# Kernel tuning notes

Hardware: AMD Instinct MI355X
Metric: run time of the kernel (lower is better)

Reference implementation:

```python
import jax, jax.numpy as jnp
import numpy as np

DIM = 2048
N_HEADS = 16
N_KV_HEADS = 8
HEAD_DIM = DIM // N_HEADS  # 128
N_REP = N_HEADS // N_KV_HEADS  # 2
HIDDEN = 4 * DIM  # Project hidden dim
SEQ = 2048
BSZ = 2
ROPE_THETA = 10000.0
NEG_INF = -1e9


def setup_inputs() -> dict:
    key = jax.random.key(0)
    ks = jax.random.split(key, 10)
    s_in = 1.0 / np.sqrt(DIM)
    s_hid = 1.0 / np.sqrt(HIDDEN)
    x = jax.random.normal(ks[0], (BSZ, SEQ, DIM), jnp.float32)
    wq = jax.random.normal(ks[1], (DIM, N_HEADS * HEAD_DIM), jnp.float32) * s_in
    wk_w1 = jax.random.normal(ks[2], (DIM, HIDDEN), jnp.float32) * s_in
    wk_w2 = jax.random.normal(ks[3], (HIDDEN, N_KV_HEADS * HEAD_DIM), jnp.float32) * s_hid
    wk_w3 = jax.random.normal(ks[4], (DIM, HIDDEN), jnp.float32) * s_in
    wv_w1 = jax.random.normal(ks[5], (DIM, HIDDEN), jnp.float32) * s_in
    wv_w2 = jax.random.normal(ks[6], (HIDDEN, N_KV_HEADS * HEAD_DIM), jnp.float32) * s_hid
    wv_w3 = jax.random.normal(ks[7], (DIM, HIDDEN), jnp.float32) * s_in
    wo = jax.random.normal(ks[8], (N_HEADS * HEAD_DIM, DIM), jnp.float32) * s_in
    # RoPE tables: angle[t, j] = t * theta^(-2j/head_dim), j in [0, head_dim/2)
    inv_freq = 1.0 / (ROPE_THETA ** (np.arange(0, HEAD_DIM, 2, dtype=np.float64) / HEAD_DIM))
    ang = np.outer(np.arange(SEQ, dtype=np.float64), inv_freq)
    freqs_cos = jnp.asarray(np.cos(ang), jnp.float32)  # [SEQ, HEAD_DIM//2]
    freqs_sin = jnp.asarray(np.sin(ang), jnp.float32)
    # causal additive mask [1, 1, SEQ, SEQ]
    mask = jnp.triu(jnp.full((SEQ, SEQ), NEG_INF, jnp.float32), k=1)[None, None]
    return {
        "x": x, "wq": wq,
        "wk_w1": wk_w1, "wk_w2": wk_w2, "wk_w3": wk_w3,
        "wv_w1": wv_w1, "wv_w2": wv_w2, "wv_w3": wv_w3,
        "wo": wo, "freqs_cos": freqs_cos, "freqs_sin": freqs_sin,
        "mask": mask, "start_pos": 0,
    }


def _rope(x, cos, sin):
    # x: [b, s, h, d]; pairs (x[2j], x[2j+1]) rotated as complex multiply
    xr = x[..., 0::2]
    xi = x[..., 1::2]
    c = cos[None, :, None, :]
    s = sin[None, :, None, :]
    out_r = xr * c - xi * s
    out_i = xr * s + xi * c
    return jnp.stack([out_r, out_i], axis=-1).reshape(x.shape)


def _project(x, w1, w2, w3):
    # SwiGLU-style projection: w2(silu(x@w1) * (x@w3))
    return (jax.nn.silu(x @ w1) * (x @ w3)) @ w2


def reference(x, wq, wk_w1, wk_w2, wk_w3, wv_w1, wv_w2, wv_w3, wo,
              freqs_cos, freqs_sin, mask, start_pos):
    b, s, _ = x.shape
    q = (x @ wq).reshape(b, s, N_HEADS, HEAD_DIM)
    q = _rope(q, freqs_cos, freqs_sin)
    k = _project(x, wk_w1, wk_w2, wk_w3).reshape(b, s, N_KV_HEADS, HEAD_DIM)
    v = _project(x, wv_w1, wv_w2, wv_w3).reshape(b, s, N_KV_HEADS, HEAD_DIM)
    k = _rope(k, freqs_cos, freqs_sin)
    o_keys, o_values = k, v  # is_training=True path: cache is just current k/v
    # repeat_kv (GQA) -> [b, h, s, d]
    kr = jnp.repeat(k, N_REP, axis=2).transpose(0, 2, 1, 3)
    vr = jnp.repeat(v, N_REP, axis=2).transpose(0, 2, 1, 3)
    qt = q.transpose(0, 2, 1, 3)
    scores = jnp.einsum('bhqd,bhkd->bhqk', qt, kr) / np.sqrt(HEAD_DIM).astype(np.float32)
    scores = scores + mask
    attn = jax.nn.softmax(scores.astype(jnp.float32), axis=-1).astype(qt.dtype)
    out = jnp.einsum('bhqk,bhkd->bhqd', attn, vr)
    out = out.transpose(0, 2, 1, 3).reshape(b, s, N_HEADS * HEAD_DIM)
    return (out @ wo, o_keys, o_values)
```

## Files before the change

### kernel.cpp

```cpp
#include <hip/hip_runtime.h>

typedef unsigned short ushort_t;
typedef __attribute__((ext_vector_type(4))) float f32x4;
typedef __attribute__((ext_vector_type(8))) __bf16 bf16x8;
typedef __attribute__((ext_vector_type(4))) unsigned short ushort4_t;
typedef __attribute__((ext_vector_type(8))) unsigned short ushort8_t;
typedef __attribute__((ext_vector_type(2))) unsigned int u32x2;

#define AS1 __attribute__((address_space(1)))
#define AS3 __attribute__((address_space(3)))

__device__ __forceinline__ float bf2f(ushort_t u) {
  unsigned int v = ((unsigned int)u) << 16;
  return __builtin_bit_cast(float, v);
}
__device__ __forceinline__ ushort_t f2bf(float f) {
  unsigned int u = __builtin_bit_cast(unsigned int, f);
  u += 0x7fffu + ((u >> 16) & 1u);
  return (ushort_t)(u >> 16);
}
__device__ __forceinline__ void storeC(float* p, float v) { *p = v; }
__device__ __forceinline__ void storeC(ushort_t* p, float v) { *p = f2bf(v); }

__global__ __launch_bounds__(256) void cast_f32_bf16(const float* __restrict__ in,
                                                     ushort_t* __restrict__ outp) {
  size_t i = ((size_t)blockIdx.x * 256 + threadIdx.x) * 4;
  f32x4 v = *(const f32x4*)(const void*)&in[i];
  ushort4_t o;
#pragma unroll
  for (int j = 0; j < 4; ++j) o[j] = f2bf(v[j]);
  *(ushort4_t*)(void*)&outp[i] = o;
}

__global__ __launch_bounds__(256) void transpose_cast_b(
    const float* __restrict__ W0, const float* __restrict__ W1,
    const float* __restrict__ W2, const float* __restrict__ W3,
    ushort_t* __restrict__ Wt, int K, int N, long long strT) {
  __shared__ float tile[32][33];
  const int z = blockIdx.z;
  const float* W = (z == 0) ? W0 : (z == 1) ? W1 : (z == 2) ? W2 : W3;
  ushort_t* out = Wt + (size_t)(strT * z);
  int n0 = blockIdx.x * 32, k0 = blockIdx.y * 32;
  int tx = threadIdx.x, ty = threadIdx.y;
#pragma unroll
  for (int i = 0; i < 4; ++i)
    tile[ty + 8 * i][tx] = W[(size_t)(k0 + ty + 8 * i) * N + n0 + tx];
  __syncthreads();
#pragma unroll
  for (int i = 0; i < 4; ++i)
    out[(size_t)(n0 + ty + 8 * i) * K + k0 + tx] = f2bf(tile[tx][ty + 8 * i]);
}

__global__ __launch_bounds__(256) void silu_mul(ushort_t* __restrict__ h1,
                                                const ushort_t* __restrict__ h3) {
  size_t i = ((size_t)blockIdx.x * 256 + threadIdx.x) * 8;
  ushort8_t a = *(const ushort8_t*)(const void*)&h1[i];
  ushort8_t b = *(const ushort8_t*)(const void*)&h3[i];
#pragma unroll
  for (int j = 0; j < 8; ++j) {
    float x = bf2f(a[j]);
    float g = x / (1.0f + __expf(-x));
    a[j] = f2bf(g * bf2f(b[j]));
  }
  *(ushort8_t*)(void*)&h1[i] = a;
}

__global__ __launch_bounds__(256) void reduce_q(const float* __restrict__ part,
                                                ushort_t* __restrict__ qb,
                                                const float* __restrict__ fc,
                                                const float* __restrict__ fs) {
  const float alpha = 0.08838834764831845f;
  int p = blockIdx.x * 256 + threadIdx.x;
  int i = p & 63;
  int row = p >> 10;
  int s = row & 2047;
  size_t src = (size_t)row * 2048 + ((p >> 6) & 15) * 128 + 2 * i;
  float xr = part[src] + part[src + 8388608];
  float xi = part[src + 1] + part[src + 8388609];
  float c = fc[s * 64 + i] * alpha, sn = fs[s * 64 + i] * alpha;
  qb[src] = f2bf(xr * c - xi * sn);
  qb[src + 1] = f2bf(xr * sn + xi * c);
}

__global__ __launch_bounds__(256) void reduce_k(const float* __restrict__ part,
                                                ushort_t* __restrict__ kb,
                                                float* __restrict__ okeys,
                                                const float* __restrict__ fc,
                                                const float* __restrict__ fs) {
  int p = blockIdx.x * 256 + threadIdx.x;
  int i = p & 63;
  int row = p >> 9;
  int s = row & 2047;
  size_t src = (size_t)row * 1024 + ((p >> 6) & 7) * 128 + 2 * i;
  float xr = part[src] + part[src + 4194304] + part[src + 8388608] + part[src + 12582912];
  float xi = part[src + 1] + part[src + 1 + 4194304] + part[src + 1 + 8388608] +
             part[src + 1 + 12582912];
  float c = fc[s * 64 + i], sn = fs[s * 64 + i];
  float orr = xr * c - xi * sn;
  float oi = xr * sn + xi * c;
  kb[src] = f2bf(orr);
  kb[src + 1] = f2bf(oi);
  okeys[src] = orr;
  okeys[src + 1] = oi;
}

__global__ __launch_bounds__(256) void reduce_v(const float* __restrict__ part,
                                                float* __restrict__ ovals,
                                                ushort_t* __restrict__ vbT) {
  __shared__ ushort_t tile[32][33];
  int s0 = blockIdx.x * 32, d0 = blockIdx.y * 32, bk = blockIdx.z;
  int b = bk >> 3, kh = bk & 7;
  int tx = threadIdx.x, ty = threadIdx.y;
#pragma unroll
  for (int i = 0; i < 4; ++i) {
    int s = s0 + ty + 8 * i;
    size_t src = ((size_t)(b * 2048 + s)) * 1024 + kh * 128 + d0 + tx;
    float v = part[src] + part[src + 4194304] + part[src + 8388608] + part[src + 12582912];
    tile[ty + 8 * i][tx] = f2bf(v);
    ovals[src] = v;
  }
  __syncthreads();
#pragma unroll
  for (int i = 0; i < 4; ++i) {
    int d = d0 + ty + 8 * i;
    vbT[((size_t)bk * 128 + d) * 2048 + s0 + tx] = tile[tx][ty + 8 * i];
  }
}

__global__ __launch_bounds__(256) void reduce_wo(const float* __restrict__ part,
                                                 float* __restrict__ outp) {
  size_t i = ((size_t)blockIdx.x * 256 + threadIdx.x) * 4;
  f32x4 a = *(const f32x4*)(const void*)&part[i];
  f32x4 b = *(const f32x4*)(const void*)&part[i + 8388608];
  *(f32x4*)(void*)&outp[i] = a + b;
}

__global__ __launch_bounds__(256) void flash_attn(
    const ushort_t* __restrict__ Q, const ushort_t* __restrict__ Kg,
    const ushort_t* __restrict__ VT, ushort_t* __restrict__ O) {
  __shared__ __align__(16) char smem[81920];
  const int xp = blockIdx.x;
  const int bh = blockIdx.y;
  const int b = bh >> 4, h = bh & 15, kh = h >> 1;
  const int t = threadIdx.x, w = t >> 6, lane = t & 63;
  const int fr = lane & 15, fh = lane >> 4;
  const size_t kelem0 = ((size_t)b * 2048) * 1024 + kh * 128;
  const size_t velem0 = ((size_t)(b * 8 + kh)) * 128 * 2048;
  const size_t qrow0 = (size_t)b * 2048;

  size_t oK[4], oV[4];
#pragma unroll
  for (int qv = 0; qv < 4; ++qv) {
    int row = w * 16 + qv * 4 + (lane >> 4);
    oK[qv] = (size_t)row * 1024 + (((lane & 15) ^ (row & 7)) * 8);
    int rd = w * 32 + qv * 8 + (lane >> 3);
    oV[qv] = (size_t)rd * 2048 + (((lane & 7) ^ (rd & 7)) * 8);
  }

  auto stage = [&](int tile, int buf) {
    const size_t kc = (size_t)tile * 64 * 1024;
    const int vc = tile * 64;
    char* kd = smem + buf * 16384 + w * 4096;
    char* vd = smem + 32768 + buf * 16384 + w * 4096;
#pragma unroll
    for (int qv = 0; qv < 4; ++qv) {
      __builtin_amdgcn_global_load_lds((const AS1 void*)(Kg + kelem0 + kc + oK[qv]),
                                       (AS3 void*)(kd + qv * 1024), 16, 0, 0);
      __builtin_amdgcn_global_load_lds((const AS1 void*)(VT + velem0 + oV[qv] + vc),
                                       (AS3 void*)(vd + qv * 1024), 16, 0, 0);
    }
  };

#pragma unroll 1
  for (int ph = 0; ph < 2; ++ph) {
    const int qi = ph ? (15 - xp) : xp;
    const int qw = qi * 128 + w * 32;
    const int nt = 2 * qi + 2;

    bf16x8 qF[2][4];
#pragma unroll
    for (int qt = 0; qt < 2; ++qt)
#pragma unroll
      for (int i = 0; i < 4; ++i)
        qF[qt][i] = *(const bf16x8*)(const void*)(
            Q + (qrow0 + qw + qt * 16 + fr) * 2048 + h * 128 + i * 32 + fh * 8);

    f32x4 acco[8][2] = {};
    float mrun[2] = {-1e30f, -1e30f};
    float lrun[2] = {0.0f, 0.0f};

    stage(0, 0);
#pragma unroll 1
    for (int tt = 0; tt < nt; ++tt) {
      const int c0 = tt * 64;
      if (tt + 1 < nt) {
        stage(tt + 1, (tt + 1) & 1);
        asm volatile("s_waitcnt vmcnt(8)" ::: "memory");
      } else {
        asm volatile("s_waitcnt vmcnt(0)" ::: "memory");
      }
      __builtin_amdgcn_sched_barrier(0);
      __builtin_amdgcn_s_barrier();
      const char* KL = smem + (tt & 1) * 16384;
      const char* VL = smem + 32768 + (tt & 1) * 16384;
      char* PL = smem + 65536 + w * 4096;
      if (c0 <= qw + 31) {
        f32x4 sacc[2][4] = {};
#pragma unroll
        for (int i = 0; i < 4; ++i)
#pragma unroll
          for (int mt = 0; mt < 4; ++mt) {
            bf16x8 kf = *(const bf16x8*)(const void*)(
                KL + (mt * 16 + fr) * 256 + (((i * 4 + fh) ^ (fr & 7)) * 16));
            sacc[0][mt] = __builtin_amdgcn_mfma_f32_16x16x32_bf16(kf, qF[0][i], sacc[0][mt], 0, 0, 0);
            sacc[1][mt] = __builtin_amdgcn_mfma_f32_16x16x32_bf16(kf, qF[1][i], sacc[1][mt], 0, 0, 0);
          }
        if (c0 + 63 > qw) {
#pragma unroll
          for (int qt = 0; qt < 2; ++qt) {
            int qg = qw + qt * 16 + fr;
#pragma unroll
            for (int mt = 0; mt < 4; ++mt)
#pragma unroll
              for (int j = 0; j < 4; ++j)
                if (c0 + mt * 16 + fh * 4 + j > qg) sacc[qt][mt][j] = -1e30f;
          }
        }
#pragma unroll
        for (int qt = 0; qt < 2; ++qt) {
          float mt_ = -1e30f;
#pragma unroll
          for (int mt = 0; mt < 4; ++mt)
#pragma unroll
            for (int j = 0; j < 4; ++j) mt_ = fmaxf(mt_, sacc[qt][mt][j]);
          mt_ = fmaxf(mt_, __shfl_xor(mt_, 16, 64));
          mt_ = fmaxf(mt_, __shfl_xor(mt_, 32, 64));
          float mnew = fmaxf(mrun[qt], mt_);
          float corr = __expf(mrun[qt] - mnew);
          mrun[qt] = mnew;
          float ps = 0.0f;
          float pv[4][4];
#pragma unroll
          for (int mt = 0; mt < 4; ++mt)
#pragma unroll
            for (int j = 0; j < 4; ++j) {
              float pe = __expf(sacc[qt][mt][j] - mnew);
              pv[mt][j] = pe;
              ps += pe;
            }
          ps += __shfl_xor(ps, 16, 64);
          ps += __shfl_xor(ps, 32, 64);
          lrun[qt] = lrun[qt] * corr + ps;
#pragma unroll
          for (int mt = 0; mt < 4; ++mt) {
            unsigned int u0, u1;
            asm("v_cvt_pk_bf16_f32 %0, %1, %2" : "=v"(u0) : "v"(pv[mt][0]), "v"(pv[mt][1]));
            asm("v_cvt_pk_bf16_f32 %0, %1, %2" : "=v"(u1) : "v"(pv[mt][2]), "v"(pv[mt][3]));
            u32x2 val;
            val[0] = u0;
            val[1] = u1;
            *(u32x2*)(void*)(PL + qt * 2048 + fr * 128 +
                             (((2 * mt + (fh >> 1)) ^ (fr & 7)) * 16) + (fh & 1) * 8) = val;
          }
#pragma unroll
          for (int dt = 0; dt < 8; ++dt) acco[dt][qt] *= corr;
        }
        bf16x8 pf[2][2];
#pragma unroll
        for (int qt = 0; qt < 2; ++qt)
#pragma unroll
          for (int ks = 0; ks < 2; ++ks)
            pf[qt][ks] = *(const bf16x8*)(const void*)(
                PL + qt * 2048 + fr * 128 + (((ks * 4 + fh) ^ (fr & 7)) * 16));
#pragma unroll
        for (int dt = 0; dt < 8; ++dt)
#pragma unroll
          for (int ks = 0; ks < 2; ++ks) {
            bf16x8 vf = *(const bf16x8*)(const void*)(
                VL + (dt * 16 + fr) * 128 + (((ks * 4 + fh) ^ (fr & 7)) * 16));
            acco[dt][0] = __builtin_amdgcn_mfma_f32_16x16x32_bf16(vf, pf[0][ks], acco[dt][0], 0, 0, 0);
            acco[dt][1] = __builtin_amdgcn_mfma_f32_16x16x32_bf16(vf, pf[1][ks], acco[dt][1], 0, 0, 0);
          }
      }
      __builtin_amdgcn_s_barrier();
    }
#pragma unroll
    for (int qt = 0; qt < 2; ++qt) {
      float inv = 1.0f / lrun[qt];
      const size_t rb = (qrow0 + qw + qt * 16 + fr) * 2048 + h * 128;
#pragma unroll
      for (int dt = 0; dt < 8; ++dt) {
        ushort4_t o4;
#pragma unroll
        for (int j = 0; j < 4; ++j) o4[j] = f2bf(acco[dt][qt][j] * inv);
        *(ushort4_t*)(void*)(O + rb + dt * 16 + fh * 4) = o4;
      }
    }
  }
}

template <typename CT>
__global__ __launch_bounds__(512, 2) void gemm256(
    const ushort_t* __restrict__ A, const ushort_t* __restrict__ B,
    CT* __restrict__ C, int K, int lda, int ldb, int ldc,
    int nwgx, int nwg, long long strA, long long strB, long long strC) {
  __shared__ __align__(16) char smem[131072];
  const int bz = blockIdx.y;
  const int bid = blockIdx.x;
  const int swz = (bid & 7) * (nwg >> 3) + (bid >> 3);
  const int r0 = (swz / nwgx) * 256;
  const int c0 = (swz % nwgx) * 256;
  const int t = threadIdx.x, w = t >> 6, lane = t & 63;
  const int wm = w >> 2, wn = w & 3;
  const int fr = lane & 15, fh = lane >> 4;
  const int sl = (fh ^ (fr & 7)) << 4;
  const int ldsw = w * 1024;
  const int srow = t >> 3;
  const int scb = (t & 7) ^ (srow & 7);
  const int NT = K >> 6;
  const ushort_t* gA = A + strA * bz + (size_t)(r0 + srow) * lda + scb * 8;
  const ushort_t* gB = B + strB * bz + (size_t)(c0 + srow) * ldb + scb * 8;

  auto stage = [&](int tile, int isB, int h) {
    const ushort_t* g = isB ? gB : gA;
    const size_t ld = isB ? (size_t)ldb : (size_t)lda;
    char* lp = (char*)smem + (isB ? 65536 : 0) + ((tile & 1) << 15) + (h << 14) + ldsw;
    const ushort_t* src = g + (size_t)(h * 128) * ld + tile * 64;
    __builtin_amdgcn_global_load_lds((const AS1 void*)src, (AS3 void*)lp, 16, 0, 0);
    __builtin_amdgcn_global_load_lds((const AS1 void*)(src + 64 * ld),
                                     (AS3 void*)(lp + 8192), 16, 0, 0);
  };

  f32x4 acc[8][4] = {};

  stage(0, 0, 0); stage(0, 1, 0); stage(0, 0, 1); stage(0, 1, 1);
  asm volatile("s_waitcnt vmcnt(0)" ::: "memory");
  __builtin_amdgcn_sched_barrier(0);
  __builtin_amdgcn_s_barrier();
  __builtin_amdgcn_sched_barrier(0);

  const int aBase = wm * 16384 + fr * 128;
  const int bBase = 65536 + wn * 8192 + fr * 128;

  bf16x8 aX[4], aY[4], bX[4], bY[4];
  {
    const char* la0 = (const char*)smem + aBase;
    const char* lb0 = (const char*)smem + bBase;
#pragma unroll
    for (int m = 0; m < 4; ++m)
      aX[m] = *(const bf16x8*)(const void*)(la0 + m * 2048 + sl);
#pragma unroll
    for (int n = 0; n < 4; ++n)
      bX[n] = *(const bf16x8*)(const void*)(lb0 + n * 2048 + sl);
  }

  for (int kt = 0; kt < NT; ++kt) {
    const int buf = (kt & 1) << 15;
    const char* la = (const char*)smem + buf + aBase;
    const char* lb = (const char*)smem + buf + bBase;
#pragma unroll
    for (int m = 0; m < 4; ++m)
      aY[m] = *(const bf16x8*)(const void*)(la + (m + 4) * 2048 + sl);
    __builtin_amdgcn_sched_barrier(0);
    __builtin_amdgcn_s_setprio(1);
#pragma unroll
    for (int m = 0; m < 4; ++m)
#pragma unroll
      for (int n = 0; n < 4; ++n)
        acc[m][n] = __builtin_amdgcn_mfma_f32_16x16x32_bf16(aX[m], bX[n], acc[m][n], 0, 0, 0);
    __builtin_amdgcn_s_setprio(0);
    __builtin_amdgcn_sched_barrier(0);
#pragma unroll
    for (int m = 0; m < 4; ++m)
      aX[m] = *(const bf16x8*)(const void*)(la + m * 2048 + (sl ^ 64));
#pragma unroll
    for (int n = 0; n < 4; ++n)
      bY[n] = *(const bf16x8*)(const void*)(lb + n * 2048 + (sl ^ 64));
    if (kt + 1 < NT) {
      stage(kt + 1, 0, 0); stage(kt + 1, 1, 0);
      stage(kt + 1, 0, 1); stage(kt + 1, 1, 1);
    }
    __builtin_amdgcn_sched_barrier(0);
    __builtin_amdgcn_s_setprio(1);
#pragma unroll
    for (int m = 0; m < 4; ++m)
#pragma unroll
      for (int n = 0; n < 4; ++n)
        acc[m + 4][n] = __builtin_amdgcn_mfma_f32_16x16x32_bf16(aY[m], bX[n], acc[m + 4][n], 0, 0, 0);
    __builtin_amdgcn_s_setprio(0);
    __builtin_amdgcn_sched_barrier(0);
#pragma unroll
    for (int m = 0; m < 4; ++m)
      aY[m] = *(const bf16x8*)(const void*)(la + (m + 4) * 2048 + (sl ^ 64));
    __builtin_amdgcn_sched_barrier(0);
    __builtin_amdgcn_s_setprio(1);
#pragma unroll
    for (int m = 0; m < 4; ++m)
#pragma unroll
      for (int n = 0; n < 4; ++n)
        acc[m][n] = __builtin_amdgcn_mfma_f32_16x16x32_bf16(aX[m], bY[n], acc[m][n], 0, 0, 0);
    __builtin_amdgcn_s_setprio(0);
    __builtin_amdgcn_sched_barrier(0);
    __builtin_amdgcn_s_setprio(1);
#pragma unroll
    for (int m = 0; m < 4; ++m)
#pragma unroll
      for (int n = 0; n < 4; ++n)
        acc[m + 4][n] = __builtin_amdgcn_mfma_f32_16x16x32_bf16(aY[m], bY[n], acc[m + 4][n], 0, 0, 0);
    __builtin_amdgcn_s_setprio(0);
    if (kt + 1 < NT) {
      asm volatile("s_waitcnt vmcnt(0)" ::: "memory");
      __builtin_amdgcn_sched_barrier(0);
      __builtin_amdgcn_s_barrier();
      __builtin_amdgcn_sched_barrier(0);
      const int nbuf = ((kt + 1) & 1) << 15;
      const char* lan = (const char*)smem + nbuf + aBase;
      const char* lbn = (const char*)smem + nbuf + bBase;
#pragma unroll
      for (int m = 0; m < 4; ++m)
        aX[m] = *(const bf16x8*)(const void*)(lan + m * 2048 + sl);
#pragma unroll
      for (int n = 0; n < 4; ++n)
        bX[n] = *(const bf16x8*)(const void*)(lbn + n * 2048 + sl);
      __builtin_amdgcn_sched_barrier(0);
    }
  }

  CT* gC = C + strC * bz;
  const int cr = r0 + wm * 128 + fh * 4;
  const int cc = c0 + wn * 64 + fr;
#pragma unroll
  for (int m = 0; m < 8; ++m)
#pragma unroll
    for (int n = 0; n < 4; ++n)
#pragma unroll
      for (int j = 0; j < 4; ++j)
        storeC(&gC[(size_t)(cr + m * 16 + j) * ldc + cc + n * 16], acc[m][n][j]);
}

extern "C" void kernel_launch(void* const* d_in, const int* in_sizes, int n_in,
                              void* d_out, int out_size, void* d_ws, size_t ws_size,
                              hipStream_t stream) {
  const float* x = (const float*)d_in[0];
  const float* wq = (const float*)d_in[1];
  const float* wk1 = (const float*)d_in[2];
  const float* wk2 = (const float*)d_in[3];
  const float* wk3 = (const float*)d_in[4];
  const float* wv1 = (const float*)d_in[5];
  const float* wv2 = (const float*)d_in[6];
  const float* wv3 = (const float*)d_in[7];
  const float* wo = (const float*)d_in[8];
  const float* fc = (const float*)d_in[9];
  const float* fs = (const float*)d_in[10];

  float* outp = (float*)d_out;
  float* okeys = outp + 8388608;
  float* ovals = outp + 12582912;

  char* p = (char*)d_ws;
  auto alloc = [&](size_t bytes) {
    char* r = p;
    p += (bytes + 255) & ~(size_t)255;
    return r;
  };
  ushort_t* xb = (ushort_t*)alloc(8388608ull * 2);
  ushort_t* w4T = (ushort_t*)alloc(4ull * 16777216 * 2);
  ushort_t* w2T = (ushort_t*)alloc(2ull * 8388608 * 2);
  ushort_t* wqoT = (ushort_t*)alloc(2ull * 4194304 * 2);
  ushort_t* qb = (ushort_t*)alloc(8388608ull * 2);
  ushort_t* kb = (ushort_t*)alloc(4194304ull * 2);
  ushort_t* vbT = (ushort_t*)alloc(4194304ull * 2);
  ushort_t* ob = (ushort_t*)alloc(8388608ull * 2);
  char* hreg = alloc(134217728ull);
  ushort_t* h1 = (ushort_t*)hreg;
  float* part67 = (float*)(hreg + 67108864);
  float* partQO = (float*)hreg;

  ushort_t* wk1T = w4T;
  ushort_t* wk2T = w2T;
  ushort_t* wv1T = w4T + 2ull * 16777216;
  ushort_t* wv2T = w2T + 8388608;
  ushort_t* wqT = wqoT;
  ushort_t* woT = wqoT + 4194304;

  dim3 tb(32, 8);

  cast_f32_bf16<<<8192, 256, 0, stream>>>(x, xb);
  transpose_cast_b<<<dim3(256, 64, 4), tb, 0, stream>>>(wk1, wk3, wv1, wv3, w4T,
                                                        2048, 8192, 16777216);
  transpose_cast_b<<<dim3(32, 256, 2), tb, 0, stream>>>(wk2, wv2, wk2, wv2, w2T,
                                                        8192, 1024, 8388608);
  transpose_cast_b<<<dim3(64, 64, 2), tb, 0, stream>>>(wq, wo, wq, wo, wqoT,
                                                       2048, 2048, 4194304);

  gemm256<float><<<dim3(128, 2), 512, 0, stream>>>(
      xb, wqT, partQO, 1024, 2048, 2048, 2048, 8, 128, 1024, 1024, 8388608);
  reduce_q<<<16384, 256, 0, stream>>>(partQO, qb, fc, fs);

  gemm256<ushort_t><<<dim3(512, 2), 512, 0, stream>>>(
      xb, wk1T, h1, 2048, 2048, 2048, 8192, 32, 512, 0, 16777216, 33554432);
  silu_mul<<<16384, 256, 0, stream>>>(h1, h1 + 33554432);
  gemm256<float><<<dim3(64, 4), 512, 0, stream>>>(
      h1, wk2T, part67, 2048, 8192, 8192, 1024, 4, 64, 2048, 2048, 4194304);
  reduce_k<<<8192, 256, 0, stream>>>(part67, kb, okeys, fc, fs);

  gemm256<ushort_t><<<dim3(512, 2), 512, 0, stream>>>(
      xb, wv1T, h1, 2048, 2048, 2048, 8192, 32, 512, 0, 16777216, 33554432);
  silu_mul<<<16384, 256, 0, stream>>>(h1, h1 + 33554432);
  gemm256<float><<<dim3(64, 4), 512, 0, stream>>>(
      h1, wv2T, part67, 2048, 8192, 8192, 1024, 4, 64, 2048, 2048, 4194304);
  reduce_v<<<dim3(64, 4, 16), tb, 0, stream>>>(part67, ovals, vbT);

  flash_attn<<<dim3(8, 32), 256, 0, stream>>>(qb, kb, vbT, ob);

  gemm256<float><<<dim3(128, 2), 512, 0, stream>>>(
      ob, woT, partQO, 1024, 2048, 2048, 2048, 8, 128, 1024, 1024, 8388608);
  reduce_wo<<<8192, 256, 0, stream>>>(partQO, outp);

  (void)in_sizes; (void)n_in; (void)out_size; (void)ws_size;
}
```

Baseline: 1.037 ms.

## Fuse SiLU-gate into down-projection GEMM A-load and store split-K partials in bf16

Removes the separate silu_mul pass by computing silu(h1)*h3 while staging A tiles into LDS inside a new gemm256_silu kernel, loading both gate and up tiles from global memory through registers. Split-K partial sums for the Q, K and V projections are now written as bf16 instead of fp32, halving partial-buffer traffic, and the reduce kernels are vectorized to 8 elements per thread. The K/V partials reuse the w4T workspace after the first-layer weights are consumed. This trades extra A-side register loads and ALU work inside the GEMM main loop, and lower precision in the partial sums, for fewer kernel launches and less memory traffic.

```diff
diff --git a/kernel.cpp b/kernel.cpp
--- a/kernel.cpp
+++ b/kernel.cpp
@@ -51,60 +51,67 @@
     out[(size_t)(n0 + ty + 8 * i) * K + k0 + tx] = f2bf(tile[tx][ty + 8 * i]);
 }
 
-__global__ __launch_bounds__(256) void silu_mul(ushort_t* __restrict__ h1,
-                                                const ushort_t* __restrict__ h3) {
-  size_t i = ((size_t)blockIdx.x * 256 + threadIdx.x) * 8;
-  ushort8_t a = *(const ushort8_t*)(const void*)&h1[i];
-  ushort8_t b = *(const ushort8_t*)(const void*)&h3[i];
-#pragma unroll
-  for (int j = 0; j < 8; ++j) {
-    float x = bf2f(a[j]);
-    float g = x / (1.0f + __expf(-x));
-    a[j] = f2bf(g * bf2f(b[j]));
-  }
-  *(ushort8_t*)(void*)&h1[i] = a;
-}
-
-__global__ __launch_bounds__(256) void reduce_q(const float* __restrict__ part,
+__global__ __launch_bounds__(256) void reduce_q(const ushort_t* __restrict__ part,
                                                 ushort_t* __restrict__ qb,
                                                 const float* __restrict__ fc,
                                                 const float* __restrict__ fs) {
   const float alpha = 0.08838834764831845f;
   int p = blockIdx.x * 256 + threadIdx.x;
-  int i = p & 63;
-  int row = p >> 10;
-  int s = row & 2047;
-  size_t src = (size_t)row * 2048 + ((p >> 6) & 15) * 128 + 2 * i;
-  float xr = part[src] + part[src + 8388608];
-  float xi = part[src + 1] + part[src + 8388609];
-  float c = fc[s * 64 + i] * alpha, sn = fs[s * 64 + i] * alpha;
-  qb[src] = f2bf(xr * c - xi * sn);
-  qb[src + 1] = f2bf(xr * sn + xi * c);
-}
-
-__global__ __launch_bounds__(256) void reduce_k(const float* __restrict__ part,
+  size_t e0 = (size_t)p * 8;
+  int i0 = (int)((e0 & 127) >> 1);
+  int s = (int)((e0 >> 11) & 2047);
+  ushort8_t a = *(const ushort8_t*)(const void*)&part[e0];
+  ushort8_t b = *(const ushort8_t*)(const void*)&part[e0 + 8388608];
+  f32x4 c4 = *(const f32x4*)(const void*)&fc[s * 64 + i0];
+  f32x4 s4 = *(const f32x4*)(const void*)&fs[s * 64 + i0];
+  ushort8_t o;
+#pragma unroll
+  for (int j = 0; j < 4; ++j) {
+    float xr = bf2f(a[2 * j]) + bf2f(b[2 * j]);
+    float xi = bf2f(a[2 * j + 1]) + bf2f(b[2 * j + 1]);
+    float c = c4[j] * alpha, sn = s4[j] * alpha;
+    o[2 * j] = f2bf(xr * c - xi * sn);
+    o[2 * j + 1] = f2bf(xr * sn + xi * c);
+  }
+  *(ushort8_t*)(void*)&qb[e0] = o;
+}
+
+__global__ __launch_bounds__(256) void reduce_k(const ushort_t* __restrict__ part,
                                                 ushort_t* __restrict__ kb,
                                                 float* __restrict__ okeys,
                                                 const float* __restrict__ fc,
                                                 const float* __restrict__ fs) {
   int p = blockIdx.x * 256 + threadIdx.x;
-  int i = p & 63;
-  int row = p >> 9;
-  int s = row & 2047;
-  size_t src = (size_t)row * 1024 + ((p >> 6) & 7) * 128 + 2 * i;
-  float xr = part[src] + part[src + 4194304] + part[src + 8388608] + part[src + 12582912];
-  float xi = part[src + 1] + part[src + 1 + 4194304] + part[src + 1 + 8388608] +
-             part[src + 1 + 12582912];
-  float c = fc[s * 64 + i], sn = fs[s * 64 + i];
-  float orr = xr * c - xi * sn;
-  float oi = xr * sn + xi * c;
-  kb[src] = f2bf(orr);
-  kb[src + 1] = f2bf(oi);
-  okeys[src] = orr;
-  okeys[src + 1] = oi;
-}
-
-__global__ __launch_bounds__(256) void reduce_v(const float* __restrict__ part,
+  size_t e0 = (size_t)p * 8;
+  int i0 = (int)((e0 & 127) >> 1);
+  int s = (int)((e0 >> 10) & 2047);
+  ushort8_t a0 = *(const ushort8_t*)(const void*)&part[e0];
+  ushort8_t a1 = *(const ushort8_t*)(const void*)&part[e0 + 4194304];
+  ushort8_t a2 = *(const ushort8_t*)(const void*)&part[e0 + 8388608];
+  ushort8_t a3 = *(const ushort8_t*)(const void*)&part[e0 + 12582912];
+  f32x4 c4 = *(const f32x4*)(const void*)&fc[s * 64 + i0];
+  f32x4 s4 = *(const f32x4*)(const void*)&fs[s * 64 + i0];
+  ushort8_t o;
+  f32x4 ov0, ov1;
+#pragma unroll
+  for (int j = 0; j < 4; ++j) {
+    float xr = bf2f(a0[2 * j]) + bf2f(a1[2 * j]) + bf2f(a2[2 * j]) + bf2f(a3[2 * j]);
+    float xi = bf2f(a0[2 * j + 1]) + bf2f(a1[2 * j + 1]) + bf2f(a2[2 * j + 1]) +
+               bf2f(a3[2 * j + 1]);
+    float c = c4[j], sn = s4[j];
+    float orr = xr * c - xi * sn;
+    float oi = xr * sn + xi * c;
+    o[2 * j] = f2bf(orr);
+    o[2 * j + 1] = f2bf(oi);
+    if (j < 2) { ov0[2 * j] = orr; ov0[2 * j + 1] = oi; }
+    else       { ov1[2 * (j - 2)] = orr; ov1[2 * (j - 2) + 1] = oi; }
+  }
+  *(ushort8_t*)(void*)&kb[e0] = o;
+  *(f32x4*)(void*)&okeys[e0] = ov0;
+  *(f32x4*)(void*)&okeys[e0 + 4] = ov1;
+}
+
+__global__ __launch_bounds__(256) void reduce_v(const ushort_t* __restrict__ part,
                                                 float* __restrict__ ovals,
                                                 ushort_t* __restrict__ vbT) {
   __shared__ ushort_t tile[32][33];
@@ -115,7 +122,8 @@
   for (int i = 0; i < 4; ++i) {
     int s = s0 + ty + 8 * i;
     size_t src = ((size_t)(b * 2048 + s)) * 1024 + kh * 128 + d0 + tx;
-    float v = part[src] + part[src + 4194304] + part[src + 8388608] + part[src + 12582912];
+    float v = bf2f(part[src]) + bf2f(part[src + 4194304]) +
+              bf2f(part[src + 8388608]) + bf2f(part[src + 12582912]);
     tile[ty + 8 * i][tx] = f2bf(v);
     ovals[src] = v;
   }
@@ -438,6 +446,174 @@
         storeC(&gC[(size_t)(cr + m * 16 + j) * ldc + cc + n * 16], acc[m][n][j]);
 }
 
+template <typename CT>
+__global__ __launch_bounds__(512, 2) void gemm256_silu(
+    const ushort_t* __restrict__ G1, const ushort_t* __restrict__ G3,
+    const ushort_t* __restrict__ B, CT* __restrict__ C, int K, int lda, int ldb,
+    int ldc, int nwgx, int nwg, long long strA, long long strB, long long strC) {
+  __shared__ __align__(16) char smem[131072];
+  const int bz = blockIdx.y;
+  const int bid = blockIdx.x;
+  const int swz = (bid & 7) * (nwg >> 3) + (bid >> 3);
+  const int r0 = (swz / nwgx) * 256;
+  const int c0 = (swz % nwgx) * 256;
+  const int t = threadIdx.x, w = t >> 6, lane = t & 63;
+  const int wm = w >> 2, wn = w & 3;
+  const int fr = lane & 15, fh = lane >> 4;
+  const int sl = (fh ^ (fr & 7)) << 4;
+  const int ldsw = w * 1024;
+  const int srow = t >> 3;
+  const int scb = (t & 7) ^ (srow & 7);
+  const int NT = K >> 6;
+  const ushort_t* g1 = G1 + strA * bz + (size_t)(r0 + srow) * lda + scb * 8;
+  const ushort_t* g3 = G3 + strA * bz + (size_t)(r0 + srow) * lda + scb * 8;
+  const ushort_t* gB = B + strB * bz + (size_t)(c0 + srow) * ldb + scb * 8;
+
+  auto stageB = [&](int tile, int h) {
+    char* lp = (char*)smem + 65536 + ((tile & 1) << 15) + (h << 14) + ldsw;
+    const ushort_t* src = gB + (size_t)(h * 128) * ldb + tile * 64;
+    __builtin_amdgcn_global_load_lds((const AS1 void*)src, (AS3 void*)lp, 16, 0, 0);
+    __builtin_amdgcn_global_load_lds((const AS1 void*)(src + 64 * ldb),
+                                     (AS3 void*)(lp + 8192), 16, 0, 0);
+  };
+  auto loadA = [&](int tile, ushort8_t r1[4], ushort8_t r3[4]) {
+#pragma unroll
+    for (int c = 0; c < 4; ++c) {
+      const size_t off = (size_t)(((c >> 1) * 128) + ((c & 1) * 64)) * lda + tile * 64;
+      r1[c] = *(const ushort8_t*)(const void*)(g1 + off);
+      r3[c] = *(const ushort8_t*)(const void*)(g3 + off);
+    }
+  };
+  auto writeA = [&](int tile, ushort8_t r1[4], ushort8_t r3[4]) {
+#pragma unroll
+    for (int c = 0; c < 4; ++c) {
+      ushort8_t o;
+#pragma unroll
+      for (int j = 0; j < 8; ++j) {
+        float x = bf2f(r1[c][j]);
+        float g = x / (1.0f + __expf(-x));
+        o[j] = f2bf(g * bf2f(r3[c][j]));
+      }
+      char* lp = (char*)smem + ((tile & 1) << 15) + ((c >> 1) << 14) +
+                 ((c & 1) * 8192) + t * 16;
+      *(ushort8_t*)(void*)lp = o;
+    }
+  };
+
+  f32x4 acc[8][4] = {};
+  ushort8_t p1[4], p3[4];
+
+  loadA(0, p1, p3);
+  stageB(0, 0); stageB(0, 1);
+  writeA(0, p1, p3);
+  asm volatile("s_waitcnt vmcnt(0)" ::: "memory");
+  asm volatile("s_waitcnt lgkmcnt(0)" ::: "memory");
+  __builtin_amdgcn_sched_barrier(0);
+  __builtin_amdgcn_s_barrier();
+  __builtin_amdgcn_sched_barrier(0);
+
+  const int aBase = wm * 16384 + fr * 128;
+  const int bBase = 65536 + wn * 8192 + fr * 128;
+
+  bf16x8 aX[4], aY[4], bX[4], bY[4];
+  {
+    const char* la0 = (const char*)smem + aBase;
+    const char* lb0 = (const char*)smem + bBase;
+#pragma unroll
+    for (int m = 0; m < 4; ++m)
+      aX[m] = *(const bf16x8*)(const void*)(la0 + m * 2048 + sl);
+#pragma unroll
+    for (int n = 0; n < 4; ++n)
+      bX[n] = *(const bf16x8*)(const void*)(lb0 + n * 2048 + sl);
+  }
+
+  for (int kt = 0; kt < NT; ++kt) {
+    const int buf = (kt & 1) << 15;
+    const char* la = (const char*)smem + buf + aBase;
+    const char* lb = (const char*)smem + buf + bBase;
+#pragma unroll
+    for (int m = 0; m < 4; ++m)
+      aY[m] = *(const bf16x8*)(const void*)(la + (m + 4) * 2048 + sl);
+    __builtin_amdgcn_sched_barrier(0);
+    __builtin_amdgcn_s_setprio(1);
+#pragma unroll
+    for (int m = 0; m < 4; ++m)
+#pragma unroll
+      for (int n = 0; n < 4; ++n)
+        acc[m][n] = __builtin_amdgcn_mfma_f32_16x16x32_bf16(aX[m], bX[n], acc[m][n], 0, 0, 0);
+    __builtin_amdgcn_s_setprio(0);
+    __builtin_amdgcn_sched_barrier(0);
+#pragma unroll
+    for (int m = 0; m < 4; ++m)
+      aX[m] = *(const bf16x8*)(const void*)(la + m * 2048 + (sl ^ 64));
+#pragma unroll
+    for (int n = 0; n < 4; ++n)
+      bY[n] = *(const bf16x8*)(const void*)(lb + n * 2048 + (sl ^ 64));
+    if (kt + 1 < NT) {
+      loadA(kt + 1, p1, p3);
+      stageB(kt + 1, 0); stageB(kt + 1, 1);
+    }
+    __builtin_amdgcn_sched_barrier(0);
+    __builtin_amdgcn_s_setprio(1);
+#pragma unroll
+    for (int m = 0; m < 4; ++m)
+#pragma unroll
+      for (int n = 0; n < 4; ++n)
+        acc[m + 4][n] = __builtin_amdgcn_mfma_f32_16x16x32_bf16(aY[m], bX[n], acc[m + 4][n], 0, 0, 0);
+    __builtin_amdgcn_s_setprio(0);
+    __builtin_amdgcn_sched_barrier(0);
+#pragma unroll
+    for (int m = 0; m < 4; ++m)
+      aY[m] = *(const bf16x8*)(const void*)(la + (m + 4) * 2048 + (sl ^ 64));
+    __builtin_amdgcn_sched_barrier(0);
+    __builtin_amdgcn_s_setprio(1);
+#pragma unroll
+    for (int m = 0; m < 4; ++m)
+#pragma unroll
+      for (int n = 0; n < 4; ++n)
+        acc[m][n] = __builtin_amdgcn_mfma_f32_16x16x32_bf16(aX[m], bY[n], acc[m][n], 0, 0, 0);
+    __builtin_amdgcn_s_setprio(0);
+    __builtin_amdgcn_sched_barrier(0);
+    if (kt + 1 < NT) writeA(kt + 1, p1, p3);
+    __builtin_amdgcn_sched_barrier(0);
+    __builtin_amdgcn_s_setprio(1);
+#pragma unroll
+    for (int m = 0; m < 4; ++m)
+#pragma unroll
+      for (int n = 0; n < 4; ++n)
+        acc[m + 4][n] = __builtin_amdgcn_mfma_f32_16x16x32_bf16(aY[m], bY[n], acc[m + 4][n], 0, 0, 0);
+    __builtin_amdgcn_s_setprio(0);
+    if (kt + 1 < NT) {
+      asm volatile("s_waitcnt vmcnt(0)" ::: "memory");
+      asm volatile("s_waitcnt lgkmcnt(0)" ::: "memory");
+      __builtin_amdgcn_sched_barrier(0);
+      __builtin_amdgcn_s_barrier();
+      __builtin_amdgcn_sched_barrier(0);
+      const int nbuf = ((kt + 1) & 1) << 15;
+      const char* lan = (const char*)smem + nbuf + aBase;
+      const char* lbn = (const char*)smem + nbuf + bBase;
+#pragma unroll
+      for (int m = 0; m < 4; ++m)
+        aX[m] = *(const bf16x8*)(const void*)(lan + m * 2048 + sl);
+#pragma unroll
+      for (int n = 0; n < 4; ++n)
+        bX[n] = *(const bf16x8*)(const void*)(lbn + n * 2048 + sl);
+      __builtin_amdgcn_sched_barrier(0);
+    }
+  }
+
+  CT* gC = C + strC * bz;
+  const int cr = r0 + wm * 128 + fh * 4;
+  const int cc = c0 + wn * 64 + fr;
+#pragma unroll
+  for (int m = 0; m < 8; ++m)
+#pragma unroll
+    for (int n = 0; n < 4; ++n)
+#pragma unroll
+      for (int j = 0; j < 4; ++j)
+        storeC(&gC[(size_t)(cr + m * 16 + j) * ldc + cc + n * 16], acc[m][n][j]);
+}
+
 extern "C" void kernel_launch(void* const* d_in, const int* in_sizes, int n_in,
                               void* d_out, int out_size, void* d_ws, size_t ws_size,
                               hipStream_t stream) {
@@ -473,8 +649,9 @@
   ushort_t* ob = (ushort_t*)alloc(8388608ull * 2);
   char* hreg = alloc(134217728ull);
   ushort_t* h1 = (ushort_t*)hreg;
-  float* part67 = (float*)(hreg + 67108864);
-  float* partQO = (float*)hreg;
+  ushort_t* partQ16 = (ushort_t*)hreg;
+  float* partWO = (float*)hreg;
+  ushort_t* part16 = (ushort_t*)w4T;
 
   ushort_t* wk1T = w4T;
   ushort_t* wk2T = w2T;
@@ -493,29 +670,29 @@
   transpose_cast_b<<<dim3(64, 64, 2), tb, 0, stream>>>(wq, wo, wq, wo, wqoT,
                                                        2048, 2048, 4194304);
 
-  gemm256<float><<<dim3(128, 2), 512, 0, stream>>>(
-      xb, wqT, partQO, 1024, 2048, 2048, 2048, 8, 128, 1024, 1024, 8388608);
-  reduce_q<<<16384, 256, 0, stream>>>(partQO, qb, fc, fs);
+  gemm256<ushort_t><<<dim3(128, 2), 512, 0, stream>>>(
+      xb, wqT, partQ16, 1024, 2048, 2048, 2048, 8, 128, 1024, 1024, 8388608);
+  reduce_q<<<4096, 256, 0, stream>>>(partQ16, qb, fc, fs);
 
   gemm256<ushort_t><<<dim3(512, 2), 512, 0, stream>>>(
       xb, wk1T, h1, 2048, 2048, 2048, 8192, 32, 512, 0, 16777216, 33554432);
-  silu_mul<<<16384, 256, 0, stream>>>(h1, h1 + 33554432);
-  gemm256<float><<<dim3(64, 4), 512, 0, stream>>>(
-      h1, wk2T, part67, 2048, 8192, 8192, 1024, 4, 64, 2048, 2048, 4194304);
-  reduce_k<<<8192, 256, 0, stream>>>(part67, kb, okeys, fc, fs);
+  gemm256_silu<ushort_t><<<dim3(64, 4), 512, 0, stream>>>(
+      h1, h1 + 33554432, wk2T, part16, 2048, 8192, 8192, 1024, 4, 64, 2048,
+      2048, 4194304);
+  reduce_k<<<2048, 256, 0, stream>>>(part16, kb, okeys, fc, fs);
 
   gemm256<ushort_t><<<dim3(512, 2), 512, 0, stream>>>(
       xb, wv1T, h1, 2048, 2048, 2048, 8192, 32, 512, 0, 16777216, 33554432);
-  silu_mul<<<16384, 256, 0, stream>>>(h1, h1 + 33554432);
-  gemm256<float><<<dim3(64, 4), 512, 0, stream>>>(
-      h1, wv2T, part67, 2048, 8192, 8192, 1024, 4, 64, 2048, 2048, 4194304);
-  reduce_v<<<dim3(64, 4, 16), tb, 0, stream>>>(part67, ovals, vbT);
+  gemm256_silu<ushort_t><<<dim3(64, 4), 512, 0, stream>>>(
+      h1, h1 + 33554432, wv2T, part16, 2048, 8192, 8192, 1024, 4, 64, 2048,
+      2048, 4194304);
+  reduce_v<<<dim3(64, 4, 16), tb, 0, stream>>>(part16, ovals, vbT);
 
   flash_attn<<<dim3(8, 32), 256, 0, stream>>>(qb, kb, vbT, ob);
 
   gemm256<float><<<dim3(128, 2), 512, 0, stream>>>(
-      ob, woT, partQO, 1024, 2048, 2048, 2048, 8, 128, 1024, 1024, 8388608);
-  reduce_wo<<<8192, 256, 0, stream>>>(partQO, outp);
+      ob, woT, partWO, 1024, 2048, 2048, 2048, 8, 128, 1024, 1024, 8388608);
+  reduce_wo<<<8192, 256, 0, stream>>>(partWO, outp);
 
   (void)in_sizes; (void)n_in; (void)out_size; (void)ws_size;
 }
```

New measurement: 1.306 ms. 25.9% more time.
